# Performance work log

Measured on AMD Instinct MI355X. Metric: run time of the kernel, lower is better.

## Reference

```python
import jax, jax.numpy as jnp
import numpy as np

B, N, T, D, H = 8, 1000, 64, 32, 4
HD = D // H
GEN_INTERVAL = 5.0


def setup_inputs() -> dict:
    key = jax.random.key(0)
    ks = jax.random.split(key, 10)
    s = 1.0 / np.sqrt(D)
    inp = {
        "x": jax.random.normal(ks[0], (B, N, T, D), dtype=jnp.float32),
        "q_w": jax.random.uniform(ks[1], (D, D), jnp.float32, -s, s),
        "q_b": jnp.zeros((D,), jnp.float32),
        "k_w": jax.random.uniform(ks[2], (D, D), jnp.float32, -s, s),
        "k_b": jnp.zeros((D,), jnp.float32),
        "v_w": jax.random.uniform(ks[3], (D, D), jnp.float32, -s, s),
        "v_b": jnp.zeros((D,), jnp.float32),
        "out_w": jax.random.uniform(ks[4], (D, D), jnp.float32, -s, s),
        "out_b": jnp.zeros((D,), jnp.float32),
        "rel_pos_bias": jax.random.uniform(ks[5], (H, T, T), jnp.float32, -s, s),
        "log_gi": jnp.array(np.log(GEN_INTERVAL), jnp.float32),
    }
    return inp


def _gi_mask(log_gi, t):
    # generation-interval weighting: gaussian around gen_int + recency term, causal
    gen_int = jnp.exp(log_gi)
    times = jnp.arange(t, dtype=jnp.float32)
    lag = times[:, None] - times[None, :]  # [T, T]
    weight = jnp.exp(-0.5 * ((lag - gen_int) / (gen_int * 0.5)) ** 2)
    recent = jnp.exp(-0.1 * jnp.abs(lag))
    mask = 0.7 * weight + 0.3 * recent
    causal = jnp.tril(jnp.ones((t, t), jnp.float32))
    return mask * causal


def reference(x, q_w, q_b, k_w, k_b, v_w, v_b, out_w, out_b, rel_pos_bias, log_gi):
    b, n, t, d = x.shape
    xf = x.reshape(b * n, t, d)
    q = (xf @ q_w + q_b).reshape(b * n, t, H, HD).transpose(0, 2, 1, 3)  # [BN,H,T,hd]
    k = (xf @ k_w + k_b).reshape(b * n, t, H, HD).transpose(0, 2, 1, 3)
    v = (xf @ v_w + v_b).reshape(b * n, t, H, HD).transpose(0, 2, 1, 3)
    scale = jnp.sqrt(jnp.asarray(HD, jnp.float32))
    attn = jnp.einsum("bhqd,bhkd->bhqk", q, k) / scale  # [BN,H,T,T]
    attn = attn + rel_pos_bias[None]
    gi = _gi_mask(log_gi, t)
    attn = attn * gi[None, None]
    attn = jax.nn.softmax(attn, axis=-1)
    out = jnp.einsum("bhqk,bhkd->bhqd", attn, v)
    out = out.transpose(0, 2, 1, 3).reshape(b * n, t, d)
    out = out @ out_w + out_b
    return out.reshape(b, n, t, d)
```

## Files before the change

### kernel.cpp

```cpp
#include <hip/hip_runtime.h>
#include <math.h>

namespace {
constexpr int T_ = 64;
constexpr int D_ = 32;

typedef _Float16 half2 __attribute__((ext_vector_type(2)));
typedef _Float16 half4 __attribute__((ext_vector_type(4)));
typedef _Float16 half8 __attribute__((ext_vector_type(8)));
typedef float f32x4 __attribute__((ext_vector_type(4)));

union H4 { half4 v4; half2 v2[2]; };
union H8 { half8 v8; half4 v4[2]; };

__global__ __launch_bounds__(256) void gia_prep(
    const float* __restrict__ qw, const float* __restrict__ kw,
    const float* __restrict__ vw, const float* __restrict__ ow,
    const float* __restrict__ rel, const float* __restrict__ lgi,
    float* __restrict__ gis32, float* __restrict__ lb32,
    _Float16* __restrict__ wimg)
{
    int t = blockIdx.x * 256 + threadIdx.x;
    const float gv = __expf(lgi[0]);
    const float LOG2E = 1.4426950408889634f;
    const float INVS  = 0.35355339059327373f;
    if (t < 1024) {
        int nt = t >> 8, mt = (t >> 6) & 3, lane = t & 63;
        int q  = (lane & 15) + 16 * nt;
        int k0 = 16 * mt + 4 * (lane >> 4);
#pragma unroll
        for (int r = 0; r < 4; ++r) {
            int k = k0 + r;
            float gi = 0.0f;
            if (k <= q) {
                float lag = (float)(q - k);
                float z = (lag - gv) / (0.5f * gv);
                gi = 0.7f * __expf(-0.5f * z * z) + 0.3f * __expf(-0.1f * lag);
            }
            gis32[t * 4 + r] = gi * INVS * LOG2E;
        }
    } else if (t < 5120) {
        int e = t - 1024;
        int h = e >> 10, nt = (e >> 8) & 3, mt = (e >> 6) & 3, lane = e & 63;
        int q  = (lane & 15) + 16 * nt;
        int k0 = 16 * mt + 4 * (lane >> 4);
#pragma unroll
        for (int r = 0; r < 4; ++r) {
            int k = k0 + r;
            float gi = 0.0f;
            if (k <= q) {
                float lag = (float)(q - k);
                float z = (lag - gv) / (0.5f * gv);
                gi = 0.7f * __expf(-0.5f * z * z) + 0.3f * __expf(-0.1f * lag);
            }
            lb32[e * 4 + r] = rel[(h * 64 + q) * 64 + k] * gi * LOG2E;
        }
    } else if (t < 7424) {
        int wi = t - 5120;
        const float* wp[4] = {qw, kw, vw, ow};
#pragma unroll
        for (int e = 0; e < 2; ++e) {
            int flat = wi * 2 + e;
            int m = flat / 1152, rem = flat % 1152;
            int c2 = rem / 36, kk = rem % 36;
            float v = (kk < 32) ? wp[m][kk * 32 + c2] : 0.0f;
            wimg[flat] = (_Float16)v;
        }
    }
}

__global__ __launch_bounds__(256, 6) void gia_main(
    const float* __restrict__ x,
    const float* __restrict__ qb_, const float* __restrict__ kb_,
    const float* __restrict__ vb_, const float* __restrict__ ob_,
    const float* __restrict__ gis32, const float* __restrict__ lb32,
    const _Float16* __restrict__ wimg,
    float* __restrict__ out)
{
    __shared__ __align__(16) _Float16 xs[64][40];
    __shared__ __align__(16) _Float16 wS[3][32][36];
    __shared__ __align__(16) _Float16 qs[64][36];
    __shared__ __align__(16) _Float16 ks_[64][36];
    __shared__ __align__(16) _Float16 vT[36][68];
    __shared__ float bS[3][32];
    __shared__ _Float16 invS[4][64];

    const int tid  = threadIdx.x;
    const int lane = tid & 63;
    const int w    = tid >> 6;
    const int l4   = lane & 15;
    const int g    = lane >> 4;
    const int bn   = blockIdx.x;

    H8 wo[2]; float obv[2];
#pragma unroll
    for (int nt = 0; nt < 2; ++nt) {
        const _Float16* wp = wimg + 3 * 1152 + (l4 + 16 * nt) * 36 + 8 * g;
        wo[nt].v4[0] = *(const half4*)wp;
        wo[nt].v4[1] = *(const half4*)(wp + 4);
        obv[nt] = ob_[l4 + 16 * nt];
    }

    {
        const float4* xv = (const float4*)(x + (size_t)bn * 2048);
        float4 a = xv[2 * tid], b = xv[2 * tid + 1];
        int t = tid >> 2, c = (tid & 3) * 8;
        half8 hx;
        hx[0] = (_Float16)a.x; hx[1] = (_Float16)a.y;
        hx[2] = (_Float16)a.z; hx[3] = (_Float16)a.w;
        hx[4] = (_Float16)b.x; hx[5] = (_Float16)b.y;
        hx[6] = (_Float16)b.z; hx[7] = (_Float16)b.w;
        *(half8*)&xs[t][c] = hx;

        const uint4* wsrc = (const uint4*)wimg;
        uint4* wdst = (uint4*)&wS[0][0][0];
        wdst[tid] = wsrc[tid];
        if (tid < 176) wdst[tid + 256] = wsrc[tid + 256];

        if (tid < 128) {
            int h = tid >> 5, j = tid & 31;
            half2 o2 = {(_Float16)1.0f, (_Float16)1.0f};
            *(half2*)&vT[9 * h + 8][2 * j] = o2;
        }
        if (tid < 96) {
            int m = tid >> 5, i = tid & 31;
            const float* bp = (m == 0) ? qb_ : (m == 1) ? kb_ : vb_;
            bS[m][i] = bp[i];
        }
    }
    __syncthreads();

    {
        half8 xa = *(const half8*)&xs[16 * w + l4][8 * g];
#pragma unroll
        for (int m = 0; m < 3; ++m) {
#pragma unroll
            for (int nt = 0; nt < 2; ++nt) {
                H8 wb;
                wb.v4[0] = *(const half4*)&wS[m][l4 + 16 * nt][8 * g];
                wb.v4[1] = *(const half4*)&wS[m][l4 + 16 * nt][8 * g + 4];
                f32x4 acc = {};
                acc = __builtin_amdgcn_mfma_f32_16x16x32_f16(xa, wb.v8, acc, 0, 0, 0);
                float bb = bS[m][l4 + 16 * nt];
                if (m == 0) {
#pragma unroll
                    for (int r = 0; r < 4; ++r)
                        qs[g * 4 + r + 16 * w][l4 + 16 * nt] = (_Float16)(acc[r] + bb);
                } else if (m == 1) {
#pragma unroll
                    for (int r = 0; r < 4; ++r)
                        ks_[g * 4 + r + 16 * w][l4 + 16 * nt] = (_Float16)(acc[r] + bb);
                } else {
                    half4 pv;
#pragma unroll
                    for (int r = 0; r < 4; ++r) pv[r] = (_Float16)(acc[r] + bb);
                    int c = l4 + 16 * nt;
                    *(half4*)&vT[9 * (c >> 3) + (c & 7)][g * 4 + 16 * w] = pv;
                }
            }
        }
    }
    __syncthreads();

    {
        const int h = w;
        half4 kfr[4], qfr[4], vfr[4];
#pragma unroll
        for (int mt = 0; mt < 4; ++mt) {
            half4 v = {};
            if (g < 2) v = *(const half4*)&ks_[l4 + 16 * mt][8 * h + 4 * g];
            kfr[mt] = v;
        }
#pragma unroll
        for (int nt = 0; nt < 4; ++nt) {
            half4 v = {};
            if (g < 2) v = *(const half4*)&qs[l4 + 16 * nt][8 * h + 4 * g];
            qfr[nt] = v;
        }
        const int vrow = 9 * h + (l4 < 9 ? l4 : 8);
#pragma unroll
        for (int ks = 0; ks < 4; ++ks)
            vfr[ks] = *(const half4*)&vT[vrow][4 * g + 16 * ks];

        f32x4 oacc[4];
#pragma unroll
        for (int i = 0; i < 4; ++i) oacc[i] = (f32x4){};

#pragma unroll
        for (int nt = 0; nt < 4; ++nt) {
            f32x4 s[4];
#pragma unroll
            for (int mt = 0; mt < 4; ++mt) {
                f32x4 z = {};
                s[mt] = __builtin_amdgcn_mfma_f32_16x16x16f16(kfr[mt], qfr[nt], z, 0, 0, 0);
            }
            half4 af[4];
#pragma unroll
            for (int mt = 0; mt < 4; ++mt) {
                f32x4 g4  = *(const f32x4*)&gis32[((nt * 4 + mt) * 64 + lane) * 4];
                f32x4 lbv = *(const f32x4*)&lb32[(((h * 4 + nt) * 4 + mt) * 64 + lane) * 4];
                float t0 = fmaf(s[mt][0], g4[0], lbv[0]);
                float t1 = fmaf(s[mt][1], g4[1], lbv[1]);
                float t2 = fmaf(s[mt][2], g4[2], lbv[2]);
                float t3 = fmaf(s[mt][3], g4[3], lbv[3]);
                H4 u;
                u.v2[0] = __builtin_bit_cast(half2, __builtin_amdgcn_cvt_pkrtz(exp2f(t0), exp2f(t1)));
                u.v2[1] = __builtin_bit_cast(half2, __builtin_amdgcn_cvt_pkrtz(exp2f(t2), exp2f(t3)));
                af[mt] = u.v4;
            }
#pragma unroll
            for (int ks = 0; ks < 4; ++ks)
                oacc[nt] = __builtin_amdgcn_mfma_f32_16x16x16f16(af[ks], vfr[ks], oacc[nt], 0, 0, 0);
        }

        _Float16 (*os_)[40] = xs;
        if (l4 < 8) {
#pragma unroll
            for (int nt = 0; nt < 4; ++nt)
#pragma unroll
                for (int r = 0; r < 4; ++r)
                    os_[g * 4 + r + 16 * nt][8 * h + l4] = (_Float16)oacc[nt][r];
        } else if (l4 == 8) {
#pragma unroll
            for (int nt = 0; nt < 4; ++nt)
#pragma unroll
                for (int r = 0; r < 4; ++r)
                    invS[h][g * 4 + r + 16 * nt] = (_Float16)oacc[nt][r];
        }
    }
    __syncthreads();

    {
        _Float16 (*os_)[40] = xs;
        half4 o0 = *(const half4*)&os_[16 * w + l4][8 * g];
        half4 o1 = *(const half4*)&os_[16 * w + l4][8 * g + 4];
        float iv = 1.0f / (float)invS[g][16 * w + l4];
        _Float16 hv = (_Float16)iv;
        o0 *= (half4){hv, hv, hv, hv};
        o1 *= (half4){hv, hv, hv, hv};
        H8 oa; oa.v4[0] = o0; oa.v4[1] = o1;
        float* yout = out + (size_t)bn * 2048;
#pragma unroll
        for (int nt = 0; nt < 2; ++nt) {
            f32x4 y = {};
            y = __builtin_amdgcn_mfma_f32_16x16x32_f16(oa.v8, wo[nt].v8, y, 0, 0, 0);
#pragma unroll
            for (int r = 0; r < 4; ++r)
                yout[(g * 4 + r + 16 * w) * 32 + l4 + 16 * nt] = y[r] + obv[nt];
        }
    }
}

}

extern "C" void kernel_launch(void* const* d_in, const int* in_sizes, int n_in,
                              void* d_out, int out_size, void* d_ws, size_t ws_size,
                              hipStream_t stream)
{
    const float* x   = (const float*)d_in[0];
    const float* qw  = (const float*)d_in[1];
    const float* qb  = (const float*)d_in[2];
    const float* kw  = (const float*)d_in[3];
    const float* kb  = (const float*)d_in[4];
    const float* vw  = (const float*)d_in[5];
    const float* vb  = (const float*)d_in[6];
    const float* ow  = (const float*)d_in[7];
    const float* ob  = (const float*)d_in[8];
    const float* rel = (const float*)d_in[9];
    const float* lgi = (const float*)d_in[10];
    float* outp = (float*)d_out;

    float*    gis32 = (float*)d_ws;
    float*    lb32  = (float*)((char*)d_ws + 16384);
    _Float16* wimg  = (_Float16*)((char*)d_ws + 81920);

    const int bn_count = in_sizes[0] / (T_ * D_);

    gia_prep<<<dim3(29), dim3(256), 0, stream>>>(qw, kw, vw, ow, rel, lgi,
                                                 gis32, lb32, wimg);
    gia_main<<<dim3(bn_count), dim3(256), 0, stream>>>(
        x, qb, kb, vb, ob, gis32, lb32, wimg, outp);
}
```

Before: 65.63 us.

## Compute per-head QKV fragments in registers, drop shared staging and two barriers

The main kernel no longer stages x, the weights, Q, K and V through shared memory. The prep kernel now writes the Q/K/V weights in a per-head, per-lane MFMA fragment layout. Each wave loads x directly from global memory in fragment order and computes its head's K, Q and V fragments with MFMAs in registers, so it can feed the attention MFMAs directly. This removes most LDS traffic and two __syncthreads, and cuts shared memory to the output tile. The cost is that each wave now reads the full x tile (4x redundant global/L2 reads) and does redundant projection work with zero-padded weights.

```diff
diff --git a/kernel.cpp b/kernel.cpp
--- a/kernel.cpp
+++ b/kernel.cpp
@@ -11,14 +11,14 @@
 typedef float f32x4 __attribute__((ext_vector_type(4)));
 
 union H4 { half4 v4; half2 v2[2]; };
-union H8 { half8 v8; half4 v4[2]; };
+union H8 { half8 v8; half2 v2[4]; };
 
 __global__ __launch_bounds__(256) void gia_prep(
     const float* __restrict__ qw, const float* __restrict__ kw,
     const float* __restrict__ vw, const float* __restrict__ ow,
     const float* __restrict__ rel, const float* __restrict__ lgi,
     float* __restrict__ gis32, float* __restrict__ lb32,
-    _Float16* __restrict__ wimg)
+    _Float16* __restrict__ wfr, _Float16* __restrict__ wo_img)
 {
     int t = blockIdx.x * 256 + threadIdx.x;
     const float gv = __expf(lgi[0]);
@@ -55,17 +55,25 @@
             }
             lb32[e * 4 + r] = rel[(h * 64 + q) * 64 + k] * gi * LOG2E;
         }
-    } else if (t < 7424) {
-        int wi = t - 5120;
-        const float* wp[4] = {qw, kw, vw, ow};
-#pragma unroll
-        for (int e = 0; e < 2; ++e) {
-            int flat = wi * 2 + e;
-            int m = flat / 1152, rem = flat % 1152;
-            int c2 = rem / 36, kk = rem % 36;
-            float v = (kk < 32) ? wp[m][kk * 32 + c2] : 0.0f;
-            wimg[flat] = (_Float16)v;
-        }
+    } else if (t < 5888) {
+        int idx = t - 5120;
+        int m = idx >> 8, lane = idx & 63;
+        int h = (idx >> 6) & 3;
+        int l4 = lane & 15, gg = lane >> 4;
+        const float* wp = (m == 0) ? qw : (m == 1) ? kw : vw;
+#pragma unroll
+        for (int j = 0; j < 8; ++j) {
+            float v = (l4 < 8) ? wp[(8 * gg + j) * 32 + 8 * h + l4] : 0.0f;
+            wfr[(size_t)idx * 8 + j] = (_Float16)v;
+        }
+    } else if (t < 6016) {
+        int idx = t - 5888;
+        int nt = idx >> 6, lane = idx & 63;
+        int l4 = lane & 15, gg = lane >> 4;
+#pragma unroll
+        for (int j = 0; j < 8; ++j)
+            wo_img[(size_t)idx * 8 + j] =
+                (_Float16)ow[(8 * gg + j) * 32 + l4 + 16 * nt];
     }
 }
 
@@ -74,15 +82,10 @@
     const float* __restrict__ qb_, const float* __restrict__ kb_,
     const float* __restrict__ vb_, const float* __restrict__ ob_,
     const float* __restrict__ gis32, const float* __restrict__ lb32,
-    const _Float16* __restrict__ wimg,
+    const _Float16* __restrict__ wfr, const _Float16* __restrict__ wo_img,
     float* __restrict__ out)
 {
-    __shared__ __align__(16) _Float16 xs[64][40];
-    __shared__ __align__(16) _Float16 wS[3][32][36];
-    __shared__ __align__(16) _Float16 qs[64][36];
-    __shared__ __align__(16) _Float16 ks_[64][36];
-    __shared__ __align__(16) _Float16 vT[36][68];
-    __shared__ float bS[3][32];
+    __shared__ __align__(16) _Float16 os_[64][40];
     __shared__ _Float16 invS[4][64];
 
     const int tid  = threadIdx.x;
@@ -91,162 +94,123 @@
     const int l4   = lane & 15;
     const int g    = lane >> 4;
     const int bn   = blockIdx.x;
-
-    H8 wo[2]; float obv[2];
-#pragma unroll
-    for (int nt = 0; nt < 2; ++nt) {
-        const _Float16* wp = wimg + 3 * 1152 + (l4 + 16 * nt) * 36 + 8 * g;
-        wo[nt].v4[0] = *(const half4*)wp;
-        wo[nt].v4[1] = *(const half4*)(wp + 4);
-        obv[nt] = ob_[l4 + 16 * nt];
-    }
+    const int h    = w;
+
+    half8 wq8 = *(const half8*)&wfr[((0 * 4 + h) * 64 + lane) * 8];
+    half8 wk8 = *(const half8*)&wfr[((1 * 4 + h) * 64 + lane) * 8];
+    half8 wv8 = *(const half8*)&wfr[((2 * 4 + h) * 64 + lane) * 8];
+    float bq[4], bk[4];
+#pragma unroll
+    for (int r = 0; r < 4; ++r) {
+        bq[r] = (g < 2) ? qb_[8 * h + 4 * g + r] : 0.0f;
+        bk[r] = (g < 2) ? kb_[8 * h + 4 * g + r] : 0.0f;
+    }
+    float bv = (l4 < 8) ? vb_[8 * h + l4] : 0.0f;
+
+    const float4* xp = (const float4*)(x + (size_t)bn * 2048 + l4 * 32 + g * 8);
+    float4 xf0[4], xf1[4];
+#pragma unroll
+    for (int t = 0; t < 4; ++t) { xf0[t] = xp[t * 128]; xf1[t] = xp[t * 128 + 1]; }
+
+    half8 xa[4];
+#pragma unroll
+    for (int t = 0; t < 4; ++t) {
+        H8 u;
+        u.v2[0] = __builtin_bit_cast(half2, __builtin_amdgcn_cvt_pkrtz(xf0[t].x, xf0[t].y));
+        u.v2[1] = __builtin_bit_cast(half2, __builtin_amdgcn_cvt_pkrtz(xf0[t].z, xf0[t].w));
+        u.v2[2] = __builtin_bit_cast(half2, __builtin_amdgcn_cvt_pkrtz(xf1[t].x, xf1[t].y));
+        u.v2[3] = __builtin_bit_cast(half2, __builtin_amdgcn_cvt_pkrtz(xf1[t].z, xf1[t].w));
+        xa[t] = u.v8;
+    }
+
+    half4 kfr[4], qfr[4], vfr[4];
+#pragma unroll
+    for (int t = 0; t < 4; ++t) {
+        f32x4 z = {};
+        f32x4 c = __builtin_amdgcn_mfma_f32_16x16x32_f16(wk8, xa[t], z, 0, 0, 0);
+        H4 u;
+        u.v2[0] = __builtin_bit_cast(half2, __builtin_amdgcn_cvt_pkrtz(c[0] + bk[0], c[1] + bk[1]));
+        u.v2[1] = __builtin_bit_cast(half2, __builtin_amdgcn_cvt_pkrtz(c[2] + bk[2], c[3] + bk[3]));
+        kfr[t] = u.v4;
+    }
+#pragma unroll
+    for (int t = 0; t < 4; ++t) {
+        f32x4 z = {};
+        f32x4 c = __builtin_amdgcn_mfma_f32_16x16x32_f16(wq8, xa[t], z, 0, 0, 0);
+        H4 u;
+        u.v2[0] = __builtin_bit_cast(half2, __builtin_amdgcn_cvt_pkrtz(c[0] + bq[0], c[1] + bq[1]));
+        u.v2[1] = __builtin_bit_cast(half2, __builtin_amdgcn_cvt_pkrtz(c[2] + bq[2], c[3] + bq[3]));
+        qfr[t] = u.v4;
+    }
+#pragma unroll
+    for (int t = 0; t < 4; ++t) {
+        f32x4 z = {};
+        f32x4 c = __builtin_amdgcn_mfma_f32_16x16x32_f16(xa[t], wv8, z, 0, 0, 0);
+        H4 u;
+        u.v2[0] = __builtin_bit_cast(half2, __builtin_amdgcn_cvt_pkrtz(c[0] + bv, c[1] + bv));
+        u.v2[1] = __builtin_bit_cast(half2, __builtin_amdgcn_cvt_pkrtz(c[2] + bv, c[3] + bv));
+        half4 vv = u.v4;
+        if (l4 == 8) vv = (half4){(_Float16)1.0f, (_Float16)1.0f,
+                                  (_Float16)1.0f, (_Float16)1.0f};
+        vfr[t] = vv;
+    }
+
+#pragma unroll
+    for (int nt = 0; nt < 4; ++nt) {
+        f32x4 s[4];
+#pragma unroll
+        for (int mt = 0; mt < 4; ++mt) {
+            f32x4 z = {};
+            s[mt] = __builtin_amdgcn_mfma_f32_16x16x16f16(kfr[mt], qfr[nt], z, 0, 0, 0);
+        }
+        half4 af[4];
+#pragma unroll
+        for (int mt = 0; mt < 4; ++mt) {
+            f32x4 g4  = *(const f32x4*)&gis32[((nt * 4 + mt) * 64 + lane) * 4];
+            f32x4 lbv = *(const f32x4*)&lb32[(((h * 4 + nt) * 4 + mt) * 64 + lane) * 4];
+            float t0 = fmaf(s[mt][0], g4[0], lbv[0]);
+            float t1 = fmaf(s[mt][1], g4[1], lbv[1]);
+            float t2 = fmaf(s[mt][2], g4[2], lbv[2]);
+            float t3 = fmaf(s[mt][3], g4[3], lbv[3]);
+            H4 u;
+            u.v2[0] = __builtin_bit_cast(half2, __builtin_amdgcn_cvt_pkrtz(exp2f(t0), exp2f(t1)));
+            u.v2[1] = __builtin_bit_cast(half2, __builtin_amdgcn_cvt_pkrtz(exp2f(t2), exp2f(t3)));
+            af[mt] = u.v4;
+        }
+        f32x4 oacc = {};
+#pragma unroll
+        for (int ks = 0; ks < 4; ++ks)
+            oacc = __builtin_amdgcn_mfma_f32_16x16x16f16(af[ks], vfr[ks], oacc, 0, 0, 0);
+        if (l4 < 8) {
+#pragma unroll
+            for (int r = 0; r < 4; ++r)
+                os_[4 * g + r + 16 * nt][8 * h + l4] = (_Float16)oacc[r];
+        } else if (l4 == 8) {
+#pragma unroll
+            for (int r = 0; r < 4; ++r)
+                invS[h][4 * g + r + 16 * nt] = (_Float16)oacc[r];
+        }
+    }
+    __syncthreads();
 
     {
-        const float4* xv = (const float4*)(x + (size_t)bn * 2048);
-        float4 a = xv[2 * tid], b = xv[2 * tid + 1];
-        int t = tid >> 2, c = (tid & 3) * 8;
-        half8 hx;
-        hx[0] = (_Float16)a.x; hx[1] = (_Float16)a.y;
-        hx[2] = (_Float16)a.z; hx[3] = (_Float16)a.w;
-        hx[4] = (_Float16)b.x; hx[5] = (_Float16)b.y;
-        hx[6] = (_Float16)b.z; hx[7] = (_Float16)b.w;
-        *(half8*)&xs[t][c] = hx;
-
-        const uint4* wsrc = (const uint4*)wimg;
-        uint4* wdst = (uint4*)&wS[0][0][0];
-        wdst[tid] = wsrc[tid];
-        if (tid < 176) wdst[tid + 256] = wsrc[tid + 256];
-
-        if (tid < 128) {
-            int h = tid >> 5, j = tid & 31;
-            half2 o2 = {(_Float16)1.0f, (_Float16)1.0f};
-            *(half2*)&vT[9 * h + 8][2 * j] = o2;
-        }
-        if (tid < 96) {
-            int m = tid >> 5, i = tid & 31;
-            const float* bp = (m == 0) ? qb_ : (m == 1) ? kb_ : vb_;
-            bS[m][i] = bp[i];
-        }
-    }
-    __syncthreads();
-
-    {
-        half8 xa = *(const half8*)&xs[16 * w + l4][8 * g];
-#pragma unroll
-        for (int m = 0; m < 3; ++m) {
-#pragma unroll
-            for (int nt = 0; nt < 2; ++nt) {
-                H8 wb;
-                wb.v4[0] = *(const half4*)&wS[m][l4 + 16 * nt][8 * g];
-                wb.v4[1] = *(const half4*)&wS[m][l4 + 16 * nt][8 * g + 4];
-                f32x4 acc = {};
-                acc = __builtin_amdgcn_mfma_f32_16x16x32_f16(xa, wb.v8, acc, 0, 0, 0);
-                float bb = bS[m][l4 + 16 * nt];
-                if (m == 0) {
-#pragma unroll
-                    for (int r = 0; r < 4; ++r)
-                        qs[g * 4 + r + 16 * w][l4 + 16 * nt] = (_Float16)(acc[r] + bb);
-                } else if (m == 1) {
-#pragma unroll
-                    for (int r = 0; r < 4; ++r)
-                        ks_[g * 4 + r + 16 * w][l4 + 16 * nt] = (_Float16)(acc[r] + bb);
-                } else {
-                    half4 pv;
-#pragma unroll
-                    for (int r = 0; r < 4; ++r) pv[r] = (_Float16)(acc[r] + bb);
-                    int c = l4 + 16 * nt;
-                    *(half4*)&vT[9 * (c >> 3) + (c & 7)][g * 4 + 16 * w] = pv;
-                }
-            }
-        }
-    }
-    __syncthreads();
-
-    {
-        const int h = w;
-        half4 kfr[4], qfr[4], vfr[4];
-#pragma unroll
-        for (int mt = 0; mt < 4; ++mt) {
-            half4 v = {};
-            if (g < 2) v = *(const half4*)&ks_[l4 + 16 * mt][8 * h + 4 * g];
-            kfr[mt] = v;
-        }
-#pragma unroll
-        for (int nt = 0; nt < 4; ++nt) {
-            half4 v = {};
-            if (g < 2) v = *(const half4*)&qs[l4 + 16 * nt][8 * h + 4 * g];
-            qfr[nt] = v;
-        }
-        const int vrow = 9 * h + (l4 < 9 ? l4 : 8);
-#pragma unroll
-        for (int ks = 0; ks < 4; ++ks)
-            vfr[ks] = *(const half4*)&vT[vrow][4 * g + 16 * ks];
-
-        f32x4 oacc[4];
-#pragma unroll
-        for (int i = 0; i < 4; ++i) oacc[i] = (f32x4){};
-
-#pragma unroll
-        for (int nt = 0; nt < 4; ++nt) {
-            f32x4 s[4];
-#pragma unroll
-            for (int mt = 0; mt < 4; ++mt) {
-                f32x4 z = {};
-                s[mt] = __builtin_amdgcn_mfma_f32_16x16x16f16(kfr[mt], qfr[nt], z, 0, 0, 0);
-            }
-            half4 af[4];
-#pragma unroll
-            for (int mt = 0; mt < 4; ++mt) {
-                f32x4 g4  = *(const f32x4*)&gis32[((nt * 4 + mt) * 64 + lane) * 4];
-                f32x4 lbv = *(const f32x4*)&lb32[(((h * 4 + nt) * 4 + mt) * 64 + lane) * 4];
-                float t0 = fmaf(s[mt][0], g4[0], lbv[0]);
-                float t1 = fmaf(s[mt][1], g4[1], lbv[1]);
-                float t2 = fmaf(s[mt][2], g4[2], lbv[2]);
-                float t3 = fmaf(s[mt][3], g4[3], lbv[3]);
-                H4 u;
-                u.v2[0] = __builtin_bit_cast(half2, __builtin_amdgcn_cvt_pkrtz(exp2f(t0), exp2f(t1)));
-                u.v2[1] = __builtin_bit_cast(half2, __builtin_amdgcn_cvt_pkrtz(exp2f(t2), exp2f(t3)));
-                af[mt] = u.v4;
-            }
-#pragma unroll
-            for (int ks = 0; ks < 4; ++ks)
-                oacc[nt] = __builtin_amdgcn_mfma_f32_16x16x16f16(af[ks], vfr[ks], oacc[nt], 0, 0, 0);
-        }
-
-        _Float16 (*os_)[40] = xs;
-        if (l4 < 8) {
-#pragma unroll
-            for (int nt = 0; nt < 4; ++nt)
-#pragma unroll
-                for (int r = 0; r < 4; ++r)
-                    os_[g * 4 + r + 16 * nt][8 * h + l4] = (_Float16)oacc[nt][r];
-        } else if (l4 == 8) {
-#pragma unroll
-            for (int nt = 0; nt < 4; ++nt)
-#pragma unroll
-                for (int r = 0; r < 4; ++r)
-                    invS[h][g * 4 + r + 16 * nt] = (_Float16)oacc[nt][r];
-        }
-    }
-    __syncthreads();
-
-    {
-        _Float16 (*os_)[40] = xs;
-        half4 o0 = *(const half4*)&os_[16 * w + l4][8 * g];
-        half4 o1 = *(const half4*)&os_[16 * w + l4][8 * g + 4];
+        half8 wo0 = *(const half8*)&wo_img[(0 * 64 + lane) * 8];
+        half8 wo1 = *(const half8*)&wo_img[(1 * 64 + lane) * 8];
+        float obv0 = ob_[l4], obv1 = ob_[l4 + 16];
+
+        half8 oa = *(const half8*)&os_[16 * w + l4][8 * g];
         float iv = 1.0f / (float)invS[g][16 * w + l4];
         _Float16 hv = (_Float16)iv;
-        o0 *= (half4){hv, hv, hv, hv};
-        o1 *= (half4){hv, hv, hv, hv};
-        H8 oa; oa.v4[0] = o0; oa.v4[1] = o1;
+        oa *= (half8){hv, hv, hv, hv, hv, hv, hv, hv};
+
         float* yout = out + (size_t)bn * 2048;
-#pragma unroll
-        for (int nt = 0; nt < 2; ++nt) {
-            f32x4 y = {};
-            y = __builtin_amdgcn_mfma_f32_16x16x32_f16(oa.v8, wo[nt].v8, y, 0, 0, 0);
-#pragma unroll
-            for (int r = 0; r < 4; ++r)
-                yout[(g * 4 + r + 16 * w) * 32 + l4 + 16 * nt] = y[r] + obv[nt];
+        f32x4 z0 = {}, z1 = {};
+        f32x4 y0 = __builtin_amdgcn_mfma_f32_16x16x32_f16(oa, wo0, z0, 0, 0, 0);
+        f32x4 y1 = __builtin_amdgcn_mfma_f32_16x16x32_f16(oa, wo1, z1, 0, 0, 0);
+#pragma unroll
+        for (int r = 0; r < 4; ++r) {
+            yout[(16 * w + 4 * g + r) * 32 + l4]      = y0[r] + obv0;
+            yout[(16 * w + 4 * g + r) * 32 + l4 + 16] = y1[r] + obv1;
         }
     }
 }
@@ -270,14 +234,15 @@
     const float* lgi = (const float*)d_in[10];
     float* outp = (float*)d_out;
 
-    float*    gis32 = (float*)d_ws;
-    float*    lb32  = (float*)((char*)d_ws + 16384);
-    _Float16* wimg  = (_Float16*)((char*)d_ws + 81920);
+    float*    gis32  = (float*)d_ws;
+    float*    lb32   = (float*)((char*)d_ws + 16384);
+    _Float16* wfr    = (_Float16*)((char*)d_ws + 81920);
+    _Float16* wo_img = (_Float16*)((char*)d_ws + 94208);
 
     const int bn_count = in_sizes[0] / (T_ * D_);
 
-    gia_prep<<<dim3(29), dim3(256), 0, stream>>>(qw, kw, vw, ow, rel, lgi,
-                                                 gis32, lb32, wimg);
+    gia_prep<<<dim3(24), dim3(256), 0, stream>>>(qw, kw, vw, ow, rel, lgi,
+                                                 gis32, lb32, wfr, wo_img);
     gia_main<<<dim3(bn_count), dim3(256), 0, stream>>>(
-        x, qb, kb, vb, ob, gis32, lb32, wimg, outp);
-}
+        x, qb, kb, vb, ob, gis32, lb32, wfr, wo_img, outp);
+}
```

Result: slower. 82.18 us (+25.2%).
